# Kernel optimization log

Measured on AMD Instinct MI355X. Metric: run time of the kernel, lower is better.

Reference implementation:

```python
import jax, jax.numpy as jnp
import numpy as np

B, S_SRC, S_TGT, H, V = 32, 128, 64, 300, 32000


def setup_inputs() -> dict:
    key = jax.random.key(0)
    ks = jax.random.split(key, 16)

    def n(k, shape, scale=0.05):
        return jax.random.normal(k, shape, dtype=jnp.float32) * scale

    return {
        "x": jax.random.randint(ks[0], (B, S_SRC), 0, V),
        "y": jax.random.randint(ks[1], (B, S_TGT), 0, V),
        "h0": jax.random.normal(ks[2], (B, H), dtype=jnp.float32),  # encoder initNormState (L=1 squeezed)
        "EN": n(ks[3], (V, H)),
        "ZH": n(ks[4], (V, H)),
        "enc_Wih": n(ks[5], (H, H)),
        "enc_Whh": n(ks[6], (H, H)),
        "enc_bih": n(ks[7], (H,)),
        "enc_bhh": n(ks[8], (H,)),
        "dec_Wih": n(ks[9], (H, H)),
        "dec_Whh": n(ks[10], (H, H)),
        "dec_bih": n(ks[11], (H,)),
        "dec_bhh": n(ks[12], (H,)),
        "W_out": n(ks[13], (V, H)),
        "b_out": n(ks[14], (V,)),
    }


def reference(x, y, h0, EN, ZH, enc_Wih, enc_Whh, enc_bih, enc_bhh,
              dec_Wih, dec_Whh, dec_bih, dec_bhh, W_out, b_out):
    # ---- encoder: 1-layer tanh RNN over source embeddings ----
    xe = EN[x]  # [B, S_src, H]

    def enc_step(h, xt):  # xt: [B, H]
        h = jnp.tanh(xt @ enc_Wih.T + enc_bih + h @ enc_Whh.T + enc_bhh)
        return h, None

    c, _ = jax.lax.scan(enc_step, h0, jnp.swapaxes(xe, 0, 1))  # c: [B, H] final hidden

    # ---- decoder: original loop always feeds encoder state c (never the updated
    # hidden) to the RNNCell; with teacher forcing (start_TF_rate=1.0) every step
    # uses y_in[t], so all T steps vectorize into one batched computation. ----
    ye = ZH[y]  # [B, T, H]
    dec_state_term = c @ dec_Whh.T + dec_bhh  # [B, H], shared across all steps
    h_dec = jnp.tanh(ye @ dec_Wih.T + dec_bih + dec_state_term[:, None, :])  # [B, T, H]
    out = h_dec @ W_out.T + b_out  # [B, T, V]
    return out
```

## Files before the change

### kernel.cpp

```cpp
#include <hip/hip_runtime.h>
#include <hip/hip_bf16.h>
#include <stdint.h>

#define BB 32
#define S_SRC 128
#define S_TGT 64
#define H 300
#define VV 32000
#define M_ROWS (BB * S_TGT)
#define KP 320

typedef __attribute__((ext_vector_type(8))) __bf16 bf16x8;
typedef __attribute__((ext_vector_type(4))) float f32x4;
typedef __attribute__((ext_vector_type(4))) unsigned short u16x4;
typedef __attribute__((ext_vector_type(2))) __fp16 f16x2;

#if defined(__has_builtin)
#if __has_builtin(__builtin_amdgcn_fdot2)
#define HAVE_FDOT2 1
#endif
#endif

__device__ inline unsigned short f2bf(float f) {
    union { float f; unsigned u; } v; v.f = f;
    unsigned r = (v.u + 0x7FFF + ((v.u >> 16) & 1)) >> 16;
    return (unsigned short)r;
}

__device__ __forceinline__ float ftanh(float x) {
    float e = __builtin_amdgcn_exp2f(x * 2.8853900817779268f);
    return 1.0f - 2.0f * __builtin_amdgcn_rcpf(e + 1.0f);
}

__device__ __forceinline__ float fdot2(f16x2 a, f16x2 b, float c) {
#ifdef HAVE_FDOT2
    return __builtin_amdgcn_fdot2(a, b, c, false);
#else
    return c + (float)a.x * (float)b.x + (float)a.y * (float)b.y;
#endif
}

__device__ __forceinline__ void gl_lds16(const void* g, void* l) {
    __builtin_amdgcn_global_load_lds(
        (const __attribute__((address_space(1))) void*)g,
        (__attribute__((address_space(3))) void*)l, 16, 0, 0);
}

__global__ void transpose4(const float* W0, const float* W1, const float* W2,
                           const float* W3, float* dst) {
    const float* srcs[4] = {W0, W1, W2, W3};
    const float* src = srcs[blockIdx.z];
    float* d = dst + (size_t)blockIdx.z * (H * H);
    __shared__ float tile[32][33];
    int j0 = blockIdx.y * 32, k0 = blockIdx.x * 32;
    for (int r = threadIdx.y; r < 32; r += blockDim.y) {
        int j = j0 + r, k = k0 + threadIdx.x;
        tile[r][threadIdx.x] = (j < H && k < H) ? src[(size_t)j * H + k] : 0.f;
    }
    __syncthreads();
    for (int r = threadIdx.y; r < 32; r += blockDim.y) {
        int k = k0 + r, j = j0 + threadIdx.x;
        if (k < H && j < H) d[(size_t)k * H + j] = tile[threadIdx.x][r];
    }
}

#define RPB 8
__global__ __launch_bounds__(192) void pproj(const int* __restrict__ x,
                                             const float* __restrict__ EN,
                                             const float* __restrict__ WihT,
                                             const float* __restrict__ bih,
                                             const float* __restrict__ bhh,
                                             float* __restrict__ P) {
    __shared__ float xe[RPB][H];
    int m0 = blockIdx.x * RPB;
    int tid = threadIdx.x;
    for (int r = 0; r < RPB; ++r) {
        int idx = x[m0 + r];
        for (int c = tid; c < H; c += 192) xe[r][c] = EN[(size_t)idx * H + c];
    }
    __syncthreads();
    if (tid < 150) {
        int j = tid * 2;
        float a0[RPB], a1[RPB];
#pragma unroll
        for (int r = 0; r < RPB; ++r) { a0[r] = 0.f; a1[r] = 0.f; }
        const float* wp = WihT + j;
        for (int k = 0; k < H; ++k) {
            float2 w = *reinterpret_cast<const float2*>(wp + (size_t)k * H);
#pragma unroll
            for (int r = 0; r < RPB; ++r) {
                float xv = xe[r][k];
                a0[r] += xv * w.x; a1[r] += xv * w.y;
            }
        }
        float b0 = bih[j] + bhh[j], b1 = bih[j + 1] + bhh[j + 1];
#pragma unroll
        for (int r = 0; r < RPB; ++r) {
            P[(size_t)(m0 + r) * H + j]     = a0[r] + b0;
            P[(size_t)(m0 + r) * H + j + 1] = a1[r] + b1;
        }
    }
}

#define ENC_T 512
__global__ __launch_bounds__(ENC_T, 2) void encoder3(const float* __restrict__ h0,
                                                     const float* __restrict__ P,
                                                     const float* __restrict__ Whh,
                                                     float* __restrict__ c) {
    __shared__ __align__(16) f16x2 hbuf2[160];
    __shared__ __align__(16) float part[3][304];
    int b = blockIdx.x, tid = threadIdx.x;
    int s = tid / 160;
    int jp = tid - s * 160;
    bool act = (s < 3) && (jp < 150);
    int j0 = jp * 2;
    int jq = s * 50 + jp;
    bool red = (s < 3) && (jp < 50);

    f16x2 w0[50], w1[50];
    if (act) {
        const float* p0 = Whh + (size_t)j0 * H + s * 100;
        const float* p1 = p0 + H;
#pragma unroll
        for (int i = 0; i < 25; ++i) {
            float4 f0 = *reinterpret_cast<const float4*>(p0 + i * 4);
            float4 f1 = *reinterpret_cast<const float4*>(p1 + i * 4);
            w0[2 * i]     = __builtin_amdgcn_cvt_pkrtz(f0.x, f0.y);
            w0[2 * i + 1] = __builtin_amdgcn_cvt_pkrtz(f0.z, f0.w);
            w1[2 * i]     = __builtin_amdgcn_cvt_pkrtz(f1.x, f1.y);
            w1[2 * i + 1] = __builtin_amdgcn_cvt_pkrtz(f1.z, f1.w);
        }
    }
    if (red) {
        float2 hv = *reinterpret_cast<const float2*>(h0 + (size_t)b * H + 2 * jq);
        hbuf2[jq] = __builtin_amdgcn_cvt_pkrtz(hv.x, hv.y);
    }
    __syncthreads();

    const float* Pb = P + (size_t)b * S_SRC * H;
    for (int t = 0; t < S_SRC; ++t) {
        float2 pv = make_float2(0.f, 0.f);
        if (red)
            pv = *reinterpret_cast<const float2*>(Pb + (size_t)t * H + 2 * jq);
        if (act) {
            float a0 = 0.f, a1 = 0.f;
            const uint2* hp = reinterpret_cast<const uint2*>(hbuf2 + s * 50);
#pragma unroll
            for (int i = 0; i < 25; ++i) {
                uint2 u = hp[i];
                f16x2 h0v = __builtin_bit_cast(f16x2, u.x);
                f16x2 h1v = __builtin_bit_cast(f16x2, u.y);
                a0 = fdot2(w0[2 * i], h0v, a0);
                a0 = fdot2(w0[2 * i + 1], h1v, a0);
                a1 = fdot2(w1[2 * i], h0v, a1);
                a1 = fdot2(w1[2 * i + 1], h1v, a1);
            }
            *reinterpret_cast<float2*>(&part[s][j0]) = make_float2(a0, a1);
        }
        __syncthreads();
        if (red) {
            float2 q0 = *reinterpret_cast<const float2*>(&part[0][2 * jq]);
            float2 q1 = *reinterpret_cast<const float2*>(&part[1][2 * jq]);
            float2 q2 = *reinterpret_cast<const float2*>(&part[2][2 * jq]);
            float s0 = q0.x + q1.x + q2.x + pv.x;
            float s1 = q0.y + q1.y + q2.y + pv.y;
            hbuf2[jq] = __builtin_amdgcn_cvt_pkrtz(ftanh(s0), ftanh(s1));
        }
        __syncthreads();
    }
    if (red) {
        f16x2 hv = hbuf2[jq];
        *reinterpret_cast<float2*>(c + (size_t)b * H + 2 * jq) =
            make_float2((float)hv.x, (float)hv.y);
    }
}

__global__ __launch_bounds__(192) void sdec(const float* __restrict__ c,
                                            const float* __restrict__ WhhT_d,
                                            const float* __restrict__ bih_d,
                                            const float* __restrict__ bhh_d,
                                            float* __restrict__ s2) {
    __shared__ float cl[H];
    int b = blockIdx.x, tid = threadIdx.x;
    for (int k = tid; k < H; k += 192) cl[k] = c[(size_t)b * H + k];
    __syncthreads();
    if (tid < 150) {
        int j = tid * 2;
        float a0 = 0.f, a1 = 0.f;
        const float* wp = WhhT_d + j;
        for (int k = 0; k < H; ++k) {
            float2 w = *reinterpret_cast<const float2*>(wp + (size_t)k * H);
            a0 += cl[k] * w.x; a1 += cl[k] * w.y;
        }
        s2[(size_t)b * H + j]     = a0 + bih_d[j] + bhh_d[j];
        s2[(size_t)b * H + j + 1] = a1 + bih_d[j + 1] + bhh_d[j + 1];
    }
}

__global__ __launch_bounds__(192) void hdec_k(const int* __restrict__ y,
                                              const float* __restrict__ ZH,
                                              const float* __restrict__ WihT_d,
                                              const float* __restrict__ s2,
                                              unsigned short* __restrict__ hdec) {
    __shared__ float ye[RPB][H];
    int m0 = blockIdx.x * RPB;
    int tid = threadIdx.x;
    for (int r = 0; r < RPB; ++r) {
        int idx = y[m0 + r];
        for (int c = tid; c < H; c += 192) ye[r][c] = ZH[(size_t)idx * H + c];
    }
    __syncthreads();
    if (tid < 150) {
        int j = tid * 2;
        float a0[RPB], a1[RPB];
#pragma unroll
        for (int r = 0; r < RPB; ++r) { a0[r] = 0.f; a1[r] = 0.f; }
        const float* wp = WihT_d + j;
        for (int k = 0; k < H; ++k) {
            float2 w = *reinterpret_cast<const float2*>(wp + (size_t)k * H);
#pragma unroll
            for (int r = 0; r < RPB; ++r) {
                float xv = ye[r][k];
                a0[r] += xv * w.x; a1[r] += xv * w.y;
            }
        }
#pragma unroll
        for (int r = 0; r < RPB; ++r) {
            int m = m0 + r;
            int b = m >> 6;
            float sv0 = s2[(size_t)b * H + j], sv1 = s2[(size_t)b * H + j + 1];
            hdec[(size_t)m * KP + j]     = f2bf(ftanh(a0[r] + sv0));
            hdec[(size_t)m * KP + j + 1] = f2bf(ftanh(a1[r] + sv1));
        }
    } else if (tid < 160) {
        int j = 300 + (tid - 150) * 2;
#pragma unroll
        for (int r = 0; r < RPB; ++r) {
            hdec[(size_t)(m0 + r) * KP + j]     = 0;
            hdec[(size_t)(m0 + r) * KP + j + 1] = 0;
        }
    }
}

__global__ __launch_bounds__(256) void wcvt(const float* __restrict__ W,
                                            unsigned short* __restrict__ Wb) {
    int id = blockIdx.x * 256 + threadIdx.x;
    int row = id / 80, c = id - row * 80;
    int k = c * 4;
    u16x4 o;
    if (k < H) {
        float4 f = *reinterpret_cast<const float4*>(W + (size_t)row * H + k);
        o[0] = f2bf(f.x); o[1] = f2bf(f.y); o[2] = f2bf(f.z); o[3] = f2bf(f.w);
    } else {
        o[0] = 0; o[1] = 0; o[2] = 0; o[3] = 0;
    }
    *reinterpret_cast<u16x4*>(Wb + (size_t)row * KP + k) = o;
}

__global__ __launch_bounds__(256) void gemm2(const unsigned short* __restrict__ A,
                                             const unsigned short* __restrict__ Wb,
                                             const float* __restrict__ bout,
                                             float* __restrict__ out) {
    __shared__ unsigned short Al[2][128 * 64];
    __shared__ unsigned short Blds[2][128 * 64];
    int tid = threadIdx.x;
    int lane = tid & 63, wv = tid >> 6;
    int wm = wv >> 1, wn = wv & 1;

    int orig = blockIdx.x;
    int wg = (orig & 7) * 500 + (orig >> 3);
    int mi = wg & 15, ni = wg >> 4;
    int m0 = mi * 128, n0 = ni * 128;

    int rowb = tid >> 3;
    int sc2 = (tid & 7) ^ (rowb & 7);

    f32x4 acc[4][4];
    f32x4 zero = {0.f, 0.f, 0.f, 0.f};
#pragma unroll
    for (int i = 0; i < 4; ++i)
#pragma unroll
        for (int j = 0; j < 4; ++j) acc[i][j] = zero;

#pragma unroll
    for (int i = 0; i < 4; ++i) {
        int row = i * 32 + rowb;
        gl_lds16(A + (size_t)(m0 + row) * KP + sc2 * 8, &Al[0][(i * 256 + tid) * 8]);
    }
#pragma unroll
    for (int i = 0; i < 4; ++i) {
        int row = i * 32 + rowb;
        gl_lds16(Wb + (size_t)(n0 + row) * KP + sc2 * 8, &Blds[0][(i * 256 + tid) * 8]);
    }

    for (int t = 0; t < 5; ++t) {
        __syncthreads();
        int buf = t & 1;
        if (t < 4) {
            int k0 = (t + 1) * 64, nb = buf ^ 1;
#pragma unroll
            for (int i = 0; i < 4; ++i) {
                int row = i * 32 + rowb;
                gl_lds16(A + (size_t)(m0 + row) * KP + k0 + sc2 * 8,
                         &Al[nb][(i * 256 + tid) * 8]);
            }
#pragma unroll
            for (int i = 0; i < 4; ++i) {
                int row = i * 32 + rowb;
                gl_lds16(Wb + (size_t)(n0 + row) * KP + k0 + sc2 * 8,
                         &Blds[nb][(i * 256 + tid) * 8]);
            }
        }
        bf16x8 af[2][4], bb[2][4];
#pragma unroll
        for (int ks = 0; ks < 2; ++ks)
#pragma unroll
            for (int i = 0; i < 4; ++i) {
                int ch = (ks * 4 + (lane >> 4)) ^ (lane & 7);
                int rowA = wm * 64 + i * 16 + (lane & 15);
                af[ks][i] = *reinterpret_cast<const bf16x8*>(&Al[buf][rowA * 64 + ch * 8]);
                int rowB = wn * 64 + i * 16 + (lane & 15);
                bb[ks][i] = *reinterpret_cast<const bf16x8*>(&Blds[buf][rowB * 64 + ch * 8]);
            }
#pragma unroll
        for (int ks = 0; ks < 2; ++ks)
#pragma unroll
            for (int i = 0; i < 4; ++i)
#pragma unroll
                for (int j = 0; j < 4; ++j)
                    acc[i][j] = __builtin_amdgcn_mfma_f32_16x16x32_bf16(
                        af[ks][i], bb[ks][j], acc[i][j], 0, 0, 0);
    }

#pragma unroll
    for (int j = 0; j < 4; ++j) {
        int col = n0 + wn * 64 + j * 16 + (lane & 15);
        float bo = bout[col];
#pragma unroll
        for (int i = 0; i < 4; ++i) {
            int rb = m0 + wm * 64 + i * 16 + (lane >> 4) * 4;
            f32x4 v = acc[i][j];
#pragma unroll
            for (int r = 0; r < 4; ++r)
                out[(size_t)(rb + r) * VV + col] = v[r] + bo;
        }
    }
}

#define LDSW 40
__global__ __launch_bounds__(256) void gemm_out(const unsigned short* __restrict__ A,
                                                const float* __restrict__ W,
                                                const float* __restrict__ bout,
                                                float* __restrict__ out) {
    __shared__ __align__(16) unsigned short Alds[128 * LDSW];
    __shared__ __align__(16) unsigned short Bl[128 * LDSW];
    int tid = threadIdx.x;
    int lane = tid & 63, wv = tid >> 6;
    int wm = wv >> 1, wn = wv & 1;
    int m0 = blockIdx.y * 128, n0 = blockIdx.x * 128;

    f32x4 acc[4][4];
    f32x4 zero = {0.f, 0.f, 0.f, 0.f};
#pragma unroll
    for (int i = 0; i < 4; ++i)
#pragma unroll
        for (int jj = 0; jj < 4; ++jj) acc[i][jj] = zero;

    for (int k0 = 0; k0 < KP; k0 += 32) {
#pragma unroll
        for (int s = 0; s < 2; ++s) {
            int slot = tid + s * 256;
            int row = slot >> 2, c16 = slot & 3;
            uint4 v = *reinterpret_cast<const uint4*>(
                &A[(size_t)(m0 + row) * KP + k0 + c16 * 8]);
            *reinterpret_cast<uint4*>(&Alds[row * LDSW + c16 * 8]) = v;
        }
#pragma unroll
        for (int s = 0; s < 2; ++s) {
            int slot = tid + s * 256;
            int row = slot >> 2, c8 = slot & 3;
            int k = k0 + c8 * 8;
            __align__(16) unsigned short tmp[8];
            if (k + 7 < H) {
                const float* src = &W[(size_t)(n0 + row) * H + k];
                float4 f0 = *reinterpret_cast<const float4*>(src);
                float4 f1 = *reinterpret_cast<const float4*>(src + 4);
                tmp[0] = f2bf(f0.x); tmp[1] = f2bf(f0.y);
                tmp[2] = f2bf(f0.z); tmp[3] = f2bf(f0.w);
                tmp[4] = f2bf(f1.x); tmp[5] = f2bf(f1.y);
                tmp[6] = f2bf(f1.z); tmp[7] = f2bf(f1.w);
            } else {
#pragma unroll
                for (int jv = 0; jv < 8; ++jv) {
                    int kk = k + jv;
                    tmp[jv] = (kk < H) ? f2bf(W[(size_t)(n0 + row) * H + kk])
                                       : (unsigned short)0;
                }
            }
            *reinterpret_cast<uint4*>(&Bl[row * LDSW + c8 * 8]) =
                *reinterpret_cast<const uint4*>(tmp);
        }
        __syncthreads();
        bf16x8 af[4], bfm[4];
#pragma unroll
        for (int i = 0; i < 4; ++i) {
            int row = wm * 64 + i * 16 + (lane & 15);
            af[i] = *reinterpret_cast<const bf16x8*>(&Alds[row * LDSW + (lane >> 4) * 8]);
        }
#pragma unroll
        for (int i = 0; i < 4; ++i) {
            int row = wn * 64 + i * 16 + (lane & 15);
            bfm[i] = *reinterpret_cast<const bf16x8*>(&Bl[row * LDSW + (lane >> 4) * 8]);
        }
#pragma unroll
        for (int i = 0; i < 4; ++i)
#pragma unroll
            for (int jj = 0; jj < 4; ++jj)
                acc[i][jj] = __builtin_amdgcn_mfma_f32_16x16x32_bf16(
                    af[i], bfm[jj], acc[i][jj], 0, 0, 0);
        __syncthreads();
    }
#pragma unroll
    for (int jj = 0; jj < 4; ++jj) {
        int col = n0 + wn * 64 + jj * 16 + (lane & 15);
        float bo = bout[col];
#pragma unroll
        for (int i = 0; i < 4; ++i) {
            int rb = m0 + wm * 64 + i * 16 + (lane >> 4) * 4;
            f32x4 v = acc[i][jj];
#pragma unroll
            for (int r = 0; r < 4; ++r)
                out[(size_t)(rb + r) * VV + col] = v[r] + bo;
        }
    }
}

extern "C" void kernel_launch(void* const* d_in, const int* in_sizes, int n_in,
                              void* d_out, int out_size, void* d_ws, size_t ws_size,
                              hipStream_t stream) {
    const int*   x       = (const int*)d_in[0];
    const int*   y       = (const int*)d_in[1];
    const float* h0      = (const float*)d_in[2];
    const float* EN      = (const float*)d_in[3];
    const float* ZH      = (const float*)d_in[4];
    const float* enc_Wih = (const float*)d_in[5];
    const float* enc_Whh = (const float*)d_in[6];
    const float* enc_bih = (const float*)d_in[7];
    const float* enc_bhh = (const float*)d_in[8];
    const float* dec_Wih = (const float*)d_in[9];
    const float* dec_Whh = (const float*)d_in[10];
    const float* dec_bih = (const float*)d_in[11];
    const float* dec_bhh = (const float*)d_in[12];
    const float* W_out   = (const float*)d_in[13];
    const float* b_out   = (const float*)d_in[14];
    float* out = (float*)d_out;
    char* base = (char*)d_ws;

    const size_t needA = 23307520, needB = 7742720;
    bool bigws = (ws_size >= needA);
    if (!bigws && ws_size < needB) return;

    float* WT = (float*)base;
    float* P  = (float*)(base + 1440000);
    float *c_, *s2_;
    unsigned short *hdec, *Wb = nullptr;
    if (bigws) {
        Wb   = (unsigned short*)(base + 1440000);
        c_   = (float*)(base + 21920000);
        s2_  = (float*)(base + 21958400);
        hdec = (unsigned short*)(base + 21996800);
    } else {
        c_   = (float*)(base + 6355200);
        s2_  = (float*)(base + 6393600);
        hdec = (unsigned short*)(base + 6432000);
    }

    transpose4<<<dim3(10, 10, 4), dim3(32, 8), 0, stream>>>(
        enc_Wih, enc_Whh, dec_Wih, dec_Whh, WT);
    pproj<<<(BB * S_SRC) / RPB, 192, 0, stream>>>(x, EN, WT, enc_bih, enc_bhh, P);
    encoder3<<<BB, ENC_T, 0, stream>>>(h0, P, enc_Whh, c_);
    sdec<<<BB, 192, 0, stream>>>(c_, WT + 270000, dec_bih, dec_bhh, s2_);
    hdec_k<<<M_ROWS / RPB, 192, 0, stream>>>(y, ZH, WT + 180000, s2_, hdec);
    if (bigws) {
        wcvt<<<(VV * 80) / 256, 256, 0, stream>>>(W_out, Wb);
        gemm2<<<4000, 256, 0, stream>>>(hdec, Wb, b_out, out);
    } else {
        gemm_out<<<dim3(VV / 128, M_ROWS / 128), 256, 0, stream>>>(hdec, W_out, b_out, out);
    }
}
```

Baseline: 279.8 us.

## Fuse encoder, decoder input projection and weight conversion into one concurrent kernel

Replaces the serial encoder, decoder-projection and weight-conversion launches with one heterogeneous kernel whose blocks take different roles. The decoder input projection and the bf16 conversion of W_out now run alongside the latency-bound 128-step encoder recurrence instead of after it. The encoder is reorganised so each of 600 threads handles half a row dot product, combined with a lane shuffle, using double-buffered hidden state and one barrier per step. The tanh finish moves to a small separate kernel, and scratch buffers are placed in the output tensor before the GEMM overwrites it. The cost is a wide 640-thread encoder block with 76 packed weights per thread, so register pressure is the main risk.

```diff
diff --git a/kernel.cpp b/kernel.cpp
--- a/kernel.cpp
+++ b/kernel.cpp
@@ -9,6 +9,11 @@
 #define VV 32000
 #define M_ROWS (BB * S_TGT)
 #define KP 320
+
+#define MEGA_T 640
+#define ENC_BLK 32
+#define HDEC_BLK 128
+#define WCVT_BLK 96
 
 typedef __attribute__((ext_vector_type(8))) __bf16 bf16x8;
 typedef __attribute__((ext_vector_type(4))) float f32x4;
@@ -102,82 +107,126 @@
     }
 }
 
-#define ENC_T 512
-__global__ __launch_bounds__(ENC_T, 2) void encoder3(const float* __restrict__ h0,
-                                                     const float* __restrict__ P,
-                                                     const float* __restrict__ Whh,
-                                                     float* __restrict__ c) {
-    __shared__ __align__(16) f16x2 hbuf2[160];
-    __shared__ __align__(16) float part[3][304];
-    int b = blockIdx.x, tid = threadIdx.x;
-    int s = tid / 160;
-    int jp = tid - s * 160;
-    bool act = (s < 3) && (jp < 150);
-    int j0 = jp * 2;
-    int jq = s * 50 + jp;
-    bool red = (s < 3) && (jp < 50);
-
-    f16x2 w0[50], w1[50];
-    if (act) {
-        const float* p0 = Whh + (size_t)j0 * H + s * 100;
-        const float* p1 = p0 + H;
-#pragma unroll
-        for (int i = 0; i < 25; ++i) {
-            float4 f0 = *reinterpret_cast<const float4*>(p0 + i * 4);
-            float4 f1 = *reinterpret_cast<const float4*>(p1 + i * 4);
-            w0[2 * i]     = __builtin_amdgcn_cvt_pkrtz(f0.x, f0.y);
-            w0[2 * i + 1] = __builtin_amdgcn_cvt_pkrtz(f0.z, f0.w);
-            w1[2 * i]     = __builtin_amdgcn_cvt_pkrtz(f1.x, f1.y);
-            w1[2 * i + 1] = __builtin_amdgcn_cvt_pkrtz(f1.z, f1.w);
-        }
-    }
-    if (red) {
-        float2 hv = *reinterpret_cast<const float2*>(h0 + (size_t)b * H + 2 * jq);
-        hbuf2[jq] = __builtin_amdgcn_cvt_pkrtz(hv.x, hv.y);
-    }
-    __syncthreads();
-
-    const float* Pb = P + (size_t)b * S_SRC * H;
-    for (int t = 0; t < S_SRC; ++t) {
-        float2 pv = make_float2(0.f, 0.f);
-        if (red)
-            pv = *reinterpret_cast<const float2*>(Pb + (size_t)t * H + 2 * jq);
+__global__ __launch_bounds__(MEGA_T) void mega(
+    const float* __restrict__ h0, const float* __restrict__ P,
+    const float* __restrict__ Whh, float* __restrict__ c,
+    const int* __restrict__ yv, const float* __restrict__ ZH,
+    const float* __restrict__ WihT_d, const float* __restrict__ bih_d,
+    float* __restrict__ t1,
+    const float* __restrict__ W, unsigned short* __restrict__ Wb) {
+    __shared__ union {
+        __fp16 hb[2][304];
+        float  ye[16][304];
+    } L;
+    int blk = blockIdx.x, tid = threadIdx.x;
+
+    if (blk < ENC_BLK) {
+        int b = blk;
+        bool act = tid < 600;
+        int j = tid >> 1, half = tid & 1;
+        f16x2 w[76];
         if (act) {
-            float a0 = 0.f, a1 = 0.f;
-            const uint2* hp = reinterpret_cast<const uint2*>(hbuf2 + s * 50);
-#pragma unroll
-            for (int i = 0; i < 25; ++i) {
-                uint2 u = hp[i];
-                f16x2 h0v = __builtin_bit_cast(f16x2, u.x);
-                f16x2 h1v = __builtin_bit_cast(f16x2, u.y);
-                a0 = fdot2(w0[2 * i], h0v, a0);
-                a0 = fdot2(w0[2 * i + 1], h1v, a0);
-                a1 = fdot2(w1[2 * i], h0v, a1);
-                a1 = fdot2(w1[2 * i + 1], h1v, a1);
-            }
-            *reinterpret_cast<float2*>(&part[s][j0]) = make_float2(a0, a1);
+            const float* wr = Whh + (size_t)j * H + half * 150;
+#pragma unroll
+            for (int i = 0; i < 75; ++i) {
+                float2 f = *reinterpret_cast<const float2*>(wr + 2 * i);
+                w[i] = __builtin_amdgcn_cvt_pkrtz(f.x, f.y);
+            }
+            w[75] = __builtin_amdgcn_cvt_pkrtz(0.f, 0.f);
+        }
+        if (act && half == 0) {
+            int pos = j < 150 ? j : j + 2;
+            L.hb[0][pos] = (__fp16)h0[(size_t)b * H + j];
+        }
+        if (tid >= 600 && tid < 608) {
+            int pi = tid - 600, bufi = pi >> 2, q = pi & 3;
+            int idx = (q < 2) ? (150 + q) : (302 + (q - 2));
+            L.hb[bufi][idx] = (__fp16)0.f;
         }
         __syncthreads();
-        if (red) {
-            float2 q0 = *reinterpret_cast<const float2*>(&part[0][2 * jq]);
-            float2 q1 = *reinterpret_cast<const float2*>(&part[1][2 * jq]);
-            float2 q2 = *reinterpret_cast<const float2*>(&part[2][2 * jq]);
-            float s0 = q0.x + q1.x + q2.x + pv.x;
-            float s1 = q0.y + q1.y + q2.y + pv.y;
-            hbuf2[jq] = __builtin_amdgcn_cvt_pkrtz(ftanh(s0), ftanh(s1));
+
+        const float* Pb = P + (size_t)b * S_SRC * H;
+        int cur = 0;
+        for (int t = 0; t < S_SRC; ++t) {
+            float pv = 0.f;
+            if (act && half == 0) pv = Pb[(size_t)t * H + j];
+            float tot = 0.f;
+            if (act) {
+                float a0 = 0.f, a1 = 0.f, a2 = 0.f, a3 = 0.f;
+                const uint2* hp =
+                    reinterpret_cast<const uint2*>(&L.hb[cur][half * 152]);
+#pragma unroll
+                for (int i = 0; i < 38; i += 2) {
+                    uint2 qa = hp[i];
+                    uint2 qb = hp[i + 1];
+                    a0 = fdot2(w[2 * i],     __builtin_bit_cast(f16x2, qa.x), a0);
+                    a1 = fdot2(w[2 * i + 1], __builtin_bit_cast(f16x2, qa.y), a1);
+                    a2 = fdot2(w[2 * i + 2], __builtin_bit_cast(f16x2, qb.x), a2);
+                    a3 = fdot2(w[2 * i + 3], __builtin_bit_cast(f16x2, qb.y), a3);
+                }
+                float a = (a0 + a1) + (a2 + a3);
+                tot = a + __shfl_xor(a, 1, 64);
+                if (half == 0) {
+                    float hv = ftanh(tot + pv);
+                    int pos = j < 150 ? j : j + 2;
+                    L.hb[cur ^ 1][pos] = (__fp16)hv;
+                }
+            }
+            __syncthreads();
+            cur ^= 1;
+        }
+        if (act && half == 0) {
+            int pos = j < 150 ? j : j + 2;
+            c[(size_t)b * H + j] = (float)L.hb[cur][pos];
+        }
+    } else if (blk < ENC_BLK + HDEC_BLK) {
+        int bi = blk - ENC_BLK;
+        int m0 = bi * 16;
+        for (int i = tid; i < 16 * 304; i += MEGA_T) {
+            int r = i / 304, cc = i - r * 304;
+            L.ye[r][cc] = (cc < H) ? ZH[(size_t)yv[m0 + r] * H + cc] : 0.f;
         }
         __syncthreads();
-    }
-    if (red) {
-        f16x2 hv = hbuf2[jq];
-        *reinterpret_cast<float2*>(c + (size_t)b * H + 2 * jq) =
-            make_float2((float)hv.x, (float)hv.y);
+        if (tid < 600) {
+            int rg = tid / 150, jp = tid - rg * 150, j0 = 2 * jp;
+            float a[4][2] = {};
+            const float* wp = WihT_d + j0;
+            for (int k = 0; k < H; k += 2) {
+                float2 wa = *reinterpret_cast<const float2*>(wp + (size_t)k * H);
+                float2 wb = *reinterpret_cast<const float2*>(wp + (size_t)(k + 1) * H);
+#pragma unroll
+                for (int r = 0; r < 4; ++r) {
+                    float2 x = *reinterpret_cast<const float2*>(&L.ye[rg * 4 + r][k]);
+                    a[r][0] += x.x * wa.x + x.y * wb.x;
+                    a[r][1] += x.x * wa.y + x.y * wb.y;
+                }
+            }
+            float b0 = bih_d[j0], b1 = bih_d[j0 + 1];
+#pragma unroll
+            for (int r = 0; r < 4; ++r) {
+                *reinterpret_cast<float2*>(&t1[(size_t)(m0 + rg * 4 + r) * 304 + j0]) =
+                    make_float2(a[r][0] + b0, a[r][1] + b1);
+            }
+        }
+    } else if (Wb != nullptr) {
+        for (int id = (blk - (ENC_BLK + HDEC_BLK)) * MEGA_T + tid; id < VV * 80;
+             id += WCVT_BLK * MEGA_T) {
+            int row = id / 80, cq = id - row * 80;
+            int k = cq * 4;
+            u16x4 o;
+            if (k < H) {
+                float4 f = *reinterpret_cast<const float4*>(W + (size_t)row * H + k);
+                o[0] = f2bf(f.x); o[1] = f2bf(f.y); o[2] = f2bf(f.z); o[3] = f2bf(f.w);
+            } else {
+                o[0] = 0; o[1] = 0; o[2] = 0; o[3] = 0;
+            }
+            *reinterpret_cast<u16x4*>(Wb + (size_t)row * KP + k) = o;
+        }
     }
 }
 
 __global__ __launch_bounds__(192) void sdec(const float* __restrict__ c,
                                             const float* __restrict__ WhhT_d,
-                                            const float* __restrict__ bih_d,
                                             const float* __restrict__ bhh_d,
                                             float* __restrict__ s2) {
     __shared__ float cl[H];
@@ -192,69 +241,23 @@
             float2 w = *reinterpret_cast<const float2*>(wp + (size_t)k * H);
             a0 += cl[k] * w.x; a1 += cl[k] * w.y;
         }
-        s2[(size_t)b * H + j]     = a0 + bih_d[j] + bhh_d[j];
-        s2[(size_t)b * H + j + 1] = a1 + bih_d[j + 1] + bhh_d[j + 1];
-    }
-}
-
-__global__ __launch_bounds__(192) void hdec_k(const int* __restrict__ y,
-                                              const float* __restrict__ ZH,
-                                              const float* __restrict__ WihT_d,
-                                              const float* __restrict__ s2,
-                                              unsigned short* __restrict__ hdec) {
-    __shared__ float ye[RPB][H];
-    int m0 = blockIdx.x * RPB;
-    int tid = threadIdx.x;
-    for (int r = 0; r < RPB; ++r) {
-        int idx = y[m0 + r];
-        for (int c = tid; c < H; c += 192) ye[r][c] = ZH[(size_t)idx * H + c];
-    }
-    __syncthreads();
-    if (tid < 150) {
-        int j = tid * 2;
-        float a0[RPB], a1[RPB];
-#pragma unroll
-        for (int r = 0; r < RPB; ++r) { a0[r] = 0.f; a1[r] = 0.f; }
-        const float* wp = WihT_d + j;
-        for (int k = 0; k < H; ++k) {
-            float2 w = *reinterpret_cast<const float2*>(wp + (size_t)k * H);
-#pragma unroll
-            for (int r = 0; r < RPB; ++r) {
-                float xv = ye[r][k];
-                a0[r] += xv * w.x; a1[r] += xv * w.y;
-            }
-        }
-#pragma unroll
-        for (int r = 0; r < RPB; ++r) {
-            int m = m0 + r;
-            int b = m >> 6;
-            float sv0 = s2[(size_t)b * H + j], sv1 = s2[(size_t)b * H + j + 1];
-            hdec[(size_t)m * KP + j]     = f2bf(ftanh(a0[r] + sv0));
-            hdec[(size_t)m * KP + j + 1] = f2bf(ftanh(a1[r] + sv1));
-        }
-    } else if (tid < 160) {
-        int j = 300 + (tid - 150) * 2;
-#pragma unroll
-        for (int r = 0; r < RPB; ++r) {
-            hdec[(size_t)(m0 + r) * KP + j]     = 0;
-            hdec[(size_t)(m0 + r) * KP + j + 1] = 0;
-        }
-    }
-}
-
-__global__ __launch_bounds__(256) void wcvt(const float* __restrict__ W,
-                                            unsigned short* __restrict__ Wb) {
-    int id = blockIdx.x * 256 + threadIdx.x;
-    int row = id / 80, c = id - row * 80;
-    int k = c * 4;
-    u16x4 o;
-    if (k < H) {
-        float4 f = *reinterpret_cast<const float4*>(W + (size_t)row * H + k);
-        o[0] = f2bf(f.x); o[1] = f2bf(f.y); o[2] = f2bf(f.z); o[3] = f2bf(f.w);
-    } else {
-        o[0] = 0; o[1] = 0; o[2] = 0; o[3] = 0;
-    }
-    *reinterpret_cast<u16x4*>(Wb + (size_t)row * KP + k) = o;
+        s2[(size_t)b * H + j]     = a0 + bhh_d[j];
+        s2[(size_t)b * H + j + 1] = a1 + bhh_d[j + 1];
+    }
+}
+
+__global__ __launch_bounds__(256) void hdec_fin(const float* __restrict__ t1,
+                                                const float* __restrict__ s2,
+                                                unsigned short* __restrict__ hdec) {
+    int blk = blockIdx.x, tid = threadIdx.x;
+    for (int i = tid; i < 8 * KP; i += 256) {
+        int r = i / KP, j = i - r * KP;
+        int m = blk * 8 + r, b = m >> 6;
+        unsigned short v = 0;
+        if (j < H)
+            v = f2bf(ftanh(t1[(size_t)m * 304 + j] + s2[(size_t)b * H + j]));
+        hdec[(size_t)m * KP + j] = v;
+    }
 }
 
 __global__ __launch_bounds__(256) void gemm2(const unsigned short* __restrict__ A,
@@ -456,12 +459,11 @@
     float* out = (float*)d_out;
     char* base = (char*)d_ws;
 
-    const size_t needA = 23307520, needB = 7742720;
+    const size_t needA = 23307520, needB = 2827520;
     bool bigws = (ws_size >= needA);
     if (!bigws && ws_size < needB) return;
 
     float* WT = (float*)base;
-    float* P  = (float*)(base + 1440000);
     float *c_, *s2_;
     unsigned short *hdec, *Wb = nullptr;
     if (bigws) {
@@ -470,19 +472,22 @@
         s2_  = (float*)(base + 21958400);
         hdec = (unsigned short*)(base + 21996800);
     } else {
-        c_   = (float*)(base + 6355200);
-        s2_  = (float*)(base + 6393600);
-        hdec = (unsigned short*)(base + 6432000);
-    }
+        c_   = (float*)(base + 1440000);
+        s2_  = (float*)(base + 1478400);
+        hdec = (unsigned short*)(base + 1516800);
+    }
+    float* P  = out;
+    float* t1 = out + 2000000;
 
     transpose4<<<dim3(10, 10, 4), dim3(32, 8), 0, stream>>>(
         enc_Wih, enc_Whh, dec_Wih, dec_Whh, WT);
     pproj<<<(BB * S_SRC) / RPB, 192, 0, stream>>>(x, EN, WT, enc_bih, enc_bhh, P);
-    encoder3<<<BB, ENC_T, 0, stream>>>(h0, P, enc_Whh, c_);
-    sdec<<<BB, 192, 0, stream>>>(c_, WT + 270000, dec_bih, dec_bhh, s2_);
-    hdec_k<<<M_ROWS / RPB, 192, 0, stream>>>(y, ZH, WT + 180000, s2_, hdec);
+    int mega_grid = bigws ? (ENC_BLK + HDEC_BLK + WCVT_BLK) : (ENC_BLK + HDEC_BLK);
+    mega<<<mega_grid, MEGA_T, 0, stream>>>(h0, P, enc_Whh, c_, y, ZH,
+                                           WT + 180000, dec_bih, t1, W_out, Wb);
+    sdec<<<BB, 192, 0, stream>>>(c_, WT + 270000, dec_bhh, s2_);
+    hdec_fin<<<M_ROWS / 8, 256, 0, stream>>>(t1, s2_, hdec);
     if (bigws) {
-        wcvt<<<(VV * 80) / 256, 256, 0, stream>>>(W_out, Wb);
         gemm2<<<4000, 256, 0, stream>>>(hdec, Wb, b_out, out);
     } else {
         gemm_out<<<dim3(VV / 128, M_ROWS / 128), 256, 0, stream>>>(hdec, W_out, b_out, out);
```

After: 256.5 us. -8.3%, faster.
